# Performance work log

Measured on AMD Instinct MI355X. Metric: run time of the kernel, lower is better.

Reference implementation:

```python
import jax, jax.numpy as jnp
import numpy as np

BITS = 4
MAXQ = (1 << BITS) - 1          # 15
PACK = 32 // BITS               # 8 values per int32
IN_F = 4096
OUT_F = 11008


def setup_inputs() -> dict:
    key = jax.random.key(0)
    k1, k2, k3, k4, k5 = jax.random.split(key, 5)
    x = jax.random.normal(k1, (8, IN_F), dtype=jnp.float32)
    qweight = jax.random.randint(k2, (IN_F // 32 * BITS, OUT_F), 0, 2147483647, dtype=jnp.int32)
    qzeros = jax.random.randint(k3, (1, OUT_F // 32 * BITS), 0, 2147483647, dtype=jnp.int32)
    scales = jax.random.uniform(k4, (1, OUT_F), dtype=jnp.float32, minval=1e-3, maxval=2e-2)
    bias = jax.random.normal(k5, (OUT_F,), dtype=jnp.float32)
    return {"x": x, "qweight": qweight, "qzeros": qzeros, "scales": scales, "bias": bias}


def reference(x, qweight, qzeros, scales, bias):
    # GPTQ-style unpack: each int32 packs PACK values of BITS bits, LSB first.
    shifts = jnp.arange(0, 32, BITS, dtype=jnp.int32)  # wf
    # unpack weights: (IN_F//PACK, OUT_F) -> (IN_F//PACK, PACK, OUT_F) -> (IN_F, OUT_F)
    w = (qweight[:, None, :] >> shifts[None, :, None]) & MAXQ
    w = w.reshape(IN_F, OUT_F).astype(scales.dtype)
    # unpack zeros: (1, OUT_F//PACK) -> (1, OUT_F//PACK, PACK) -> (1, OUT_F), +1 per GPTQ convention
    z = ((qzeros[:, :, None] >> shifts[None, None, :]) & MAXQ) + 1
    z = z.reshape(1, OUT_F).astype(scales.dtype)
    # single quantization group (group_size == infeatures, g_idx all zeros)
    W = scales * (w - z)                      # (IN_F, OUT_F)
    return x @ W + bias
```

## Files before the change

kernel.cpp:

```cpp
#include <hip/hip_runtime.h>

#define IN_F 4096
#define OUT_F 11008
#define M 8
#define KROWS 512
#define S_SLICES 32
#define ROWS_PER_SLICE (KROWS / S_SLICES)
#define GEMM_THREADS 128
#define NJ4 (OUT_F / 4)

__global__ __launch_bounds__(64) void rowsum_kernel(
    const float* __restrict__ x, float* __restrict__ rs)
{
    const int r = blockIdx.x;
    const int t = threadIdx.x;
    const float4* xp = (const float4*)(x + (size_t)r * IN_F);
    float s = 0.0f;
#pragma unroll
    for (int c = 0; c < 16; ++c) {
        float4 v = xp[c * 64 + t];
        s += v.x + v.y + v.z + v.w;
    }
#pragma unroll
    for (int off = 1; off < 64; off <<= 1) s += __shfl_xor(s, off, 64);
    if (t == 0) rs[r] = s;
}

__global__ __launch_bounds__(GEMM_THREADS) void gptq_gemm_partial(
    const float* __restrict__ x,
    const int*   __restrict__ qw,
    float*       __restrict__ P)
{
    const int t  = threadIdx.x;
    const int j0 = blockIdx.x * (GEMM_THREADS * 2) + 2 * t;
    const int i0 = blockIdx.y * ROWS_PER_SLICE;

    float acc[M][2];
#pragma unroll
    for (int r = 0; r < M; ++r) { acc[r][0] = 0.0f; acc[r][1] = 0.0f; }

    for (int i = 0; i < ROWS_PER_SLICE; ++i) {
        const int row = i0 + i;
        const int2 q = *(const int2*)(qw + (size_t)row * OUT_F + j0);
        const int kb = row * 8;

        float4 xa[M], xb[M];
#pragma unroll
        for (int r = 0; r < M; ++r) {
            const float* xp = x + (size_t)r * IN_F + kb;
            xa[r] = *(const float4*)xp;
            xb[r] = *(const float4*)(xp + 4);
        }

#pragma unroll
        for (int p = 0; p < 8; ++p) {
            const float w0 = (float)((q.x >> (4 * p)) & 15);
            const float w1 = (float)((q.y >> (4 * p)) & 15);
#pragma unroll
            for (int r = 0; r < M; ++r) {
                const float xv = (p < 4) ? ((const float*)&xa[r])[p]
                                         : ((const float*)&xb[r])[p - 4];
                acc[r][0] = fmaf(w0, xv, acc[r][0]);
                acc[r][1] = fmaf(w1, xv, acc[r][1]);
            }
        }
    }

    float* Pp = P + (size_t)blockIdx.y * M * OUT_F;
#pragma unroll
    for (int r = 0; r < M; ++r) {
        float2 v; v.x = acc[r][0]; v.y = acc[r][1];
        *(float2*)(Pp + (size_t)r * OUT_F + j0) = v;
    }
}

__global__ __launch_bounds__(256) void reduce_kernel(
    const float* __restrict__ P,
    const float* __restrict__ rs,
    const int*   __restrict__ qz,
    const float* __restrict__ sc,
    const float* __restrict__ bias,
    float*       __restrict__ out)
{
    const int idx = blockIdx.x * 256 + threadIdx.x;
    const int jq  = idx % NJ4;
    const int r   = idx / NJ4;
    const int j0  = jq * 4;

    float4 acc = {0.0f, 0.0f, 0.0f, 0.0f};
#pragma unroll 8
    for (int s = 0; s < S_SLICES; ++s) {
        const float4 v = *(const float4*)(P + (size_t)s * M * OUT_F + (size_t)r * OUT_F + j0);
        acc.x += v.x; acc.y += v.y; acc.z += v.z; acc.w += v.w;
    }

    const int zw = qz[j0 >> 3];
    const int sh = (j0 & 7) * 4;
    const float z0 = (float)(((zw >> (sh     )) & 15) + 1);
    const float z1 = (float)(((zw >> (sh +  4)) & 15) + 1);
    const float z2 = (float)(((zw >> (sh +  8)) & 15) + 1);
    const float z3 = (float)(((zw >> (sh + 12)) & 15) + 1);

    const float rsum = rs[r];
    const float4 s4 = *(const float4*)(sc + j0);
    const float4 b4 = *(const float4*)(bias + j0);

    float4 o;
    o.x = fmaf(s4.x, acc.x - z0 * rsum, b4.x);
    o.y = fmaf(s4.y, acc.y - z1 * rsum, b4.y);
    o.z = fmaf(s4.z, acc.z - z2 * rsum, b4.z);
    o.w = fmaf(s4.w, acc.w - z3 * rsum, b4.w);
    *(float4*)(out + (size_t)r * OUT_F + j0) = o;
}

extern "C" void kernel_launch(void* const* d_in, const int* in_sizes, int n_in,
                              void* d_out, int out_size, void* d_ws, size_t ws_size,
                              hipStream_t stream) {
    const float* x    = (const float*)d_in[0];
    const int*   qw   = (const int*)d_in[1];
    const int*   qz   = (const int*)d_in[2];
    const float* sc   = (const float*)d_in[3];
    const float* bias = (const float*)d_in[4];
    float* out = (float*)d_out;

    float* P  = (float*)d_ws;
    float* rs = P + (size_t)S_SLICES * M * OUT_F;

    hipLaunchKernelGGL(rowsum_kernel, dim3(M), dim3(64), 0, stream, x, rs);

    dim3 grid(OUT_F / (GEMM_THREADS * 2), S_SLICES);
    hipLaunchKernelGGL(gptq_gemm_partial, grid, dim3(GEMM_THREADS), 0, stream,
                       x, qw, P);

    hipLaunchKernelGGL(reduce_kernel, dim3((M * NJ4) / 256), dim3(256), 0, stream,
                       P, rs, qz, sc, bias, out);
}
```

Measured before the change: 96.62 us.

## Double split-K slices, prefetch next weight row, scalarize reduce kernel

Increases split-K slices from 32 to 64 so each GEMM block handles 8 rows, and prefetches the next packed weight row while computing the current one. The x loads are split into two half-row batches to reduce register pressure. The reduce kernel now handles one output per thread with scalar loads instead of float4. The trade-off is a doubled partial-sum buffer to write and read, plus narrower memory accesses in the reduction.

```diff
diff --git a/kernel.cpp b/kernel.cpp
--- a/kernel.cpp
+++ b/kernel.cpp
@@ -4,10 +4,9 @@
 #define OUT_F 11008
 #define M 8
 #define KROWS 512
-#define S_SLICES 32
-#define ROWS_PER_SLICE (KROWS / S_SLICES)
+#define S_SLICES 64
+#define RPS (KROWS / S_SLICES)
 #define GEMM_THREADS 128
-#define NJ4 (OUT_F / 4)
 
 __global__ __launch_bounds__(64) void rowsum_kernel(
     const float* __restrict__ x, float* __restrict__ rs)
@@ -33,45 +32,48 @@
 {
     const int t  = threadIdx.x;
     const int j0 = blockIdx.x * (GEMM_THREADS * 2) + 2 * t;
-    const int i0 = blockIdx.y * ROWS_PER_SLICE;
+    const int i0 = blockIdx.y * RPS;
 
-    float acc[M][2];
+    float2 acc[M];
 #pragma unroll
-    for (int r = 0; r < M; ++r) { acc[r][0] = 0.0f; acc[r][1] = 0.0f; }
+    for (int r = 0; r < M; ++r) { acc[r].x = 0.0f; acc[r].y = 0.0f; }
 
-    for (int i = 0; i < ROWS_PER_SLICE; ++i) {
-        const int row = i0 + i;
-        const int2 q = *(const int2*)(qw + (size_t)row * OUT_F + j0);
-        const int kb = row * 8;
-
-        float4 xa[M], xb[M];
-#pragma unroll
-        for (int r = 0; r < M; ++r) {
-            const float* xp = x + (size_t)r * IN_F + kb;
-            xa[r] = *(const float4*)xp;
-            xb[r] = *(const float4*)(xp + 4);
-        }
+    const int* qp = qw + (size_t)i0 * OUT_F + j0;
+    int2 q = *(const int2*)qp;
 
 #pragma unroll
-        for (int p = 0; p < 8; ++p) {
-            const float w0 = (float)((q.x >> (4 * p)) & 15);
-            const float w1 = (float)((q.y >> (4 * p)) & 15);
+    for (int i = 0; i < RPS; ++i) {
+        int2 qn = q;
+        if (i + 1 < RPS)
+            qn = *(const int2*)(qp + (size_t)(i + 1) * OUT_F);
+        const int kb = (i0 + i) * 8;
+
 #pragma unroll
-            for (int r = 0; r < M; ++r) {
-                const float xv = (p < 4) ? ((const float*)&xa[r])[p]
-                                         : ((const float*)&xb[r])[p - 4];
-                acc[r][0] = fmaf(w0, xv, acc[r][0]);
-                acc[r][1] = fmaf(w1, xv, acc[r][1]);
+        for (int h = 0; h < 2; ++h) {
+            float4 xv[M];
+#pragma unroll
+            for (int r = 0; r < M; ++r)
+                xv[r] = *(const float4*)(x + (size_t)r * IN_F + kb + 4 * h);
+#pragma unroll
+            for (int p = 0; p < 4; ++p) {
+                const int sh = 4 * (4 * h + p);
+                const float w0 = (float)((q.x >> sh) & 15);
+                const float w1 = (float)((q.y >> sh) & 15);
+#pragma unroll
+                for (int r = 0; r < M; ++r) {
+                    const float xs = ((const float*)&xv[r])[p];
+                    acc[r].x = fmaf(w0, xs, acc[r].x);
+                    acc[r].y = fmaf(w1, xs, acc[r].y);
+                }
             }
         }
+        q = qn;
     }
 
     float* Pp = P + (size_t)blockIdx.y * M * OUT_F;
 #pragma unroll
-    for (int r = 0; r < M; ++r) {
-        float2 v; v.x = acc[r][0]; v.y = acc[r][1];
-        *(float2*)(Pp + (size_t)r * OUT_F + j0) = v;
-    }
+    for (int r = 0; r < M; ++r)
+        *(float2*)(Pp + (size_t)r * OUT_F + j0) = acc[r];
 }
 
 __global__ __launch_bounds__(256) void reduce_kernel(
@@ -83,34 +85,18 @@
     float*       __restrict__ out)
 {
     const int idx = blockIdx.x * 256 + threadIdx.x;
-    const int jq  = idx % NJ4;
-    const int r   = idx / NJ4;
-    const int j0  = jq * 4;
+    const int j = idx % OUT_F;
+    const int r = idx / OUT_F;
 
-    float4 acc = {0.0f, 0.0f, 0.0f, 0.0f};
-#pragma unroll 8
-    for (int s = 0; s < S_SLICES; ++s) {
-        const float4 v = *(const float4*)(P + (size_t)s * M * OUT_F + (size_t)r * OUT_F + j0);
-        acc.x += v.x; acc.y += v.y; acc.z += v.z; acc.w += v.w;
-    }
+    float acc = 0.0f;
+#pragma unroll 16
+    for (int s = 0; s < S_SLICES; ++s)
+        acc += P[(size_t)s * M * OUT_F + (size_t)r * OUT_F + j];
 
-    const int zw = qz[j0 >> 3];
-    const int sh = (j0 & 7) * 4;
-    const float z0 = (float)(((zw >> (sh     )) & 15) + 1);
-    const float z1 = (float)(((zw >> (sh +  4)) & 15) + 1);
-    const float z2 = (float)(((zw >> (sh +  8)) & 15) + 1);
-    const float z3 = (float)(((zw >> (sh + 12)) & 15) + 1);
+    const int zw = qz[j >> 3];
+    const float z = (float)(((zw >> ((j & 7) * 4)) & 15) + 1);
 
-    const float rsum = rs[r];
-    const float4 s4 = *(const float4*)(sc + j0);
-    const float4 b4 = *(const float4*)(bias + j0);
-
-    float4 o;
-    o.x = fmaf(s4.x, acc.x - z0 * rsum, b4.x);
-    o.y = fmaf(s4.y, acc.y - z1 * rsum, b4.y);
-    o.z = fmaf(s4.z, acc.z - z2 * rsum, b4.z);
-    o.w = fmaf(s4.w, acc.w - z3 * rsum, b4.w);
-    *(float4*)(out + (size_t)r * OUT_F + j0) = o;
+    out[(size_t)r * OUT_F + j] = fmaf(sc[j], acc - z * rs[r], bias[j]);
 }
 
 extern "C" void kernel_launch(void* const* d_in, const int* in_sizes, int n_in,
@@ -132,6 +118,6 @@
     hipLaunchKernelGGL(gptq_gemm_partial, grid, dim3(GEMM_THREADS), 0, stream,
                        x, qw, P);
 
-    hipLaunchKernelGGL(reduce_kernel, dim3((M * NJ4) / 256), dim3(256), 0, stream,
+    hipLaunchKernelGGL(reduce_kernel, dim3((M * OUT_F) / 256), dim3(256), 0, stream,
                        P, rs, qz, sc, bias, out);
 }
```

Result: faster. 93.60 us (-3.1%).
